# Performance work log

Measured on AMD Instinct MI355X. Metric: run time of the kernel, lower is better.

Reference implementation:

```python
import jax, jax.numpy as jnp
import numpy as np

DIM = 1024
NUM_HEADS = 16
NUM_GROUPS = 8


def setup_inputs() -> dict:
    key = jax.random.key(0)
    k1, k2, k3, k4 = jax.random.split(key, 4)
    B, L = 4, 4096
    x = jax.random.normal(k1, (B, L, DIM), dtype=jnp.float32)
    # torch Linear weights: [out_features, in_features]
    w_qkv = jax.random.normal(k2, (3 * DIM, DIM), dtype=jnp.float32) * (DIM ** -0.5)
    w_out = jax.random.normal(k3, (DIM, DIM), dtype=jnp.float32) * (DIM ** -0.5)
    b_out = jax.random.normal(k4, (DIM,), dtype=jnp.float32) * 0.01
    return {"x": x, "w_qkv": w_qkv, "w_out": w_out, "b_out": b_out}


def reference(x, w_qkv, w_out, b_out):
    B, L, D = x.shape
    H, G = NUM_HEADS, NUM_GROUPS
    dh = D // H
    lg = L // G  # block length per group
    # fused QKV projection (no bias)
    qkv = x @ w_qkv.T  # [B, L, 3D]
    qkv = qkv.reshape(B, L, 3, H, dh)
    qkv = jnp.transpose(qkv, (2, 0, 3, 1, 4))  # [3, B, H, L, dh]
    q, k, v = qkv[0], qkv[1], qkv[2]
    # group sequence into G blocks of length lg; attention within each block
    q = q.reshape(B, H, G, lg, dh)
    k = k.reshape(B, H, G, lg, dh)
    v = v.reshape(B, H, G, lg, dh)
    scale = dh ** -0.5
    scores = jnp.einsum('bhgld,bhgmd->bhglm', q, k) * scale  # [B,H,G,lg,lg]
    attn = jax.nn.softmax(scores, axis=-1)
    out = jnp.einsum('bhglm,bhgmd->bhgld', attn, v)  # [B,H,G,lg,dh]
    # 'b h g l d -> b (g l) (h d)'
    out = jnp.transpose(out, (0, 2, 3, 1, 4)).reshape(B, L, D)
    return out @ w_out.T + b_out
```

## Files before the change

kernel.cpp:

```cpp
#include <hip/hip_runtime.h>
#include <hip/hip_bf16.h>
#include <stdint.h>

typedef __bf16 bf16_t;
typedef __bf16 bf16x4 __attribute__((ext_vector_type(4)));
typedef __bf16 bf16x8 __attribute__((ext_vector_type(8)));
typedef float floatx4 __attribute__((ext_vector_type(4)));

#define MFMA_16x16x32_BF16(a, b, c) __builtin_amdgcn_mfma_f32_16x16x32_bf16((a), (b), (c), 0, 0, 0)

__device__ __forceinline__ void gload_lds16(const bf16_t* g, bf16_t* lds_base) {
  __builtin_amdgcn_global_load_lds(
      (const __attribute__((address_space(1))) void*)g,
      (__attribute__((address_space(3))) void*)lds_base, 16, 0, 0);
}

__global__ __launch_bounds__(256)
void f32_to_bf16_kernel(const float* __restrict__ in, bf16_t* __restrict__ out, int n8)
{
  for (int i = blockIdx.x * 256 + threadIdx.x; i < n8; i += gridDim.x * 256) {
    const float* p = in + (size_t)i * 8;
    floatx4 f0 = *(const floatx4*)p;
    floatx4 f1 = *(const floatx4*)(p + 4);
    bf16x8 r;
#pragma unroll
    for (int j = 0; j < 4; j++) { r[j] = (bf16_t)f0[j]; r[j + 4] = (bf16_t)f1[j]; }
    *(bf16x8*)(out + (size_t)i * 8) = r;
  }
}

template <typename TOUT, bool BIAS>
__global__ __launch_bounds__(512, 1)
void gemm_bt256(const bf16_t* __restrict__ A, const bf16_t* __restrict__ B,
                const float* __restrict__ bias, TOUT* __restrict__ C,
                int M, int N, int K)
{
  __shared__ bf16_t S[65536];
  const int t = threadIdx.x;
  const int lane = t & 63, wave = t >> 6;
  const int quad = lane >> 4, l15 = lane & 15;
  const int wm = wave >> 2, wn = wave & 3;

  const int cpx = gridDim.x >> 3;
  const int obid = blockIdx.x;
  const int bid = (obid & 7) * cpx + (obid >> 3);
  const int nbx = N >> 8;
  const int bx = bid % nbx, by = bid / nbx;
  const int m0 = by * 256, n0 = bx * 256;

  uint32_t aoff[4], boff[4];
  bf16_t* asd[4]; bf16_t* bsd[4];
#pragma unroll
  for (int j = 0; j < 4; j++) {
    const uint32_t o = (uint32_t)(j * 512 + t) * 16u;
    const uint32_t u = o ^ (((o >> 7) & 7u) << 4);
    const uint32_t row = u >> 7, colb = u & 127u;
    aoff[j] = (uint32_t)(m0 + row) * (uint32_t)(K * 2) + colb;
    boff[j] = (uint32_t)(n0 + row) * (uint32_t)(K * 2) + colb;
    asd[j] = S + j * 4096 + wave * 512;
    bsd[j] = S + 32768 + j * 4096 + wave * 512;
  }

  const uint32_t sw = (uint32_t)((l15 & 7) << 4);
  const uint32_t ce0 = (((uint32_t)(quad * 16)) ^ sw) >> 1;
  const uint32_t ce1 = ce0 ^ 32u;
  const bf16_t* lraA0 = S + (wm * 128 + l15) * 64 + ce0;
  const bf16_t* lraA1 = S + (wm * 128 + l15) * 64 + ce1;
  const bf16_t* lraB0 = S + 32768 + (wn * 64 + l15) * 64 + ce0;
  const bf16_t* lraB1 = S + 32768 + (wn * 64 + l15) * 64 + ce1;

  floatx4 acc[8][4] = {};

  const int NT = K >> 6;
#pragma unroll
  for (int j = 0; j < 4; j++) gload_lds16((const bf16_t*)((const char*)A + aoff[j]), asd[j]);
#pragma unroll
  for (int j = 0; j < 4; j++) gload_lds16((const bf16_t*)((const char*)B + boff[j]), bsd[j]);
#pragma unroll
  for (int j = 0; j < 4; j++) gload_lds16((const bf16_t*)((const char*)A + aoff[j] + 128), asd[j] + 16384);
#pragma unroll
  for (int j = 0; j < 4; j++) gload_lds16((const bf16_t*)((const char*)B + boff[j] + 128), bsd[j] + 16384);

  for (int kt = 0; kt < NT; kt++) {
    const int bo = (kt & 1) * 16384;
    if (kt < NT - 1) asm volatile("s_waitcnt vmcnt(8)" ::: "memory");
    else             asm volatile("s_waitcnt vmcnt(0)" ::: "memory");
    __builtin_amdgcn_s_barrier();
    __builtin_amdgcn_sched_barrier(0);

    bf16x8 af[4][2], bA[2][2], bB[2][2];
#pragma unroll
    for (int mi = 0; mi < 4; mi++) {
      af[mi][0] = *(const bf16x8*)(lraA0 + bo + mi * 1024);
      af[mi][1] = *(const bf16x8*)(lraA1 + bo + mi * 1024);
    }
#pragma unroll
    for (int ni = 0; ni < 2; ni++) {
      bA[ni][0] = *(const bf16x8*)(lraB0 + bo + ni * 1024);
      bA[ni][1] = *(const bf16x8*)(lraB1 + bo + ni * 1024);
    }
    __builtin_amdgcn_s_setprio(1);
#pragma unroll
    for (int mi = 0; mi < 4; mi++)
#pragma unroll
      for (int ni = 0; ni < 2; ni++) {
        acc[mi][ni] = MFMA_16x16x32_BF16(af[mi][0], bA[ni][0], acc[mi][ni]);
        acc[mi][ni] = MFMA_16x16x32_BF16(af[mi][1], bA[ni][1], acc[mi][ni]);
      }
    __builtin_amdgcn_s_setprio(0);
#pragma unroll
    for (int ni = 0; ni < 2; ni++) {
      bB[ni][0] = *(const bf16x8*)(lraB0 + bo + (ni + 2) * 1024);
      bB[ni][1] = *(const bf16x8*)(lraB1 + bo + (ni + 2) * 1024);
    }
    __builtin_amdgcn_s_setprio(1);
#pragma unroll
    for (int mi = 0; mi < 4; mi++)
#pragma unroll
      for (int ni = 0; ni < 2; ni++) {
        acc[mi][ni + 2] = MFMA_16x16x32_BF16(af[mi][0], bB[ni][0], acc[mi][ni + 2]);
        acc[mi][ni + 2] = MFMA_16x16x32_BF16(af[mi][1], bB[ni][1], acc[mi][ni + 2]);
      }
    __builtin_amdgcn_s_setprio(0);
#pragma unroll
    for (int mi = 0; mi < 4; mi++) {
      af[mi][0] = *(const bf16x8*)(lraA0 + bo + (mi + 4) * 1024);
      af[mi][1] = *(const bf16x8*)(lraA1 + bo + (mi + 4) * 1024);
    }
    __builtin_amdgcn_s_setprio(1);
#pragma unroll
    for (int mi = 0; mi < 4; mi++)
#pragma unroll
      for (int ni = 0; ni < 2; ni++) {
        acc[mi + 4][ni + 2] = MFMA_16x16x32_BF16(af[mi][0], bB[ni][0], acc[mi + 4][ni + 2]);
        acc[mi + 4][ni + 2] = MFMA_16x16x32_BF16(af[mi][1], bB[ni][1], acc[mi + 4][ni + 2]);
      }
    __builtin_amdgcn_s_setprio(0);
    __builtin_amdgcn_sched_barrier(0);
    __builtin_amdgcn_s_barrier();
    __builtin_amdgcn_sched_barrier(0);
    if (kt + 2 < NT) {
      const uint32_t kadv = (uint32_t)((kt + 2) * 128);
#pragma unroll
      for (int j = 0; j < 4; j++)
        gload_lds16((const bf16_t*)((const char*)A + aoff[j] + kadv), asd[j] + bo);
#pragma unroll
      for (int j = 0; j < 4; j++)
        gload_lds16((const bf16_t*)((const char*)B + boff[j] + kadv), bsd[j] + bo);
    }
    __builtin_amdgcn_s_setprio(1);
#pragma unroll
    for (int mi = 0; mi < 4; mi++)
#pragma unroll
      for (int ni = 0; ni < 2; ni++) {
        acc[mi + 4][ni] = MFMA_16x16x32_BF16(af[mi][0], bA[ni][0], acc[mi + 4][ni]);
        acc[mi + 4][ni] = MFMA_16x16x32_BF16(af[mi][1], bA[ni][1], acc[mi + 4][ni]);
      }
    __builtin_amdgcn_s_setprio(0);
  }

  if constexpr (sizeof(TOUT) == 2) {
    __syncthreads();
    bf16_t* Sw = S + wave * 1024;
#pragma unroll
    for (int mi = 0; mi < 8; mi++) {
#pragma unroll
      for (int ni = 0; ni < 4; ni++) {
        const int col = ((ni ^ quad) & 3) * 16 + l15;
        const float bv = BIAS ? bias[n0 + wn * 64 + ni * 16 + l15] : 0.0f;
#pragma unroll
        for (int r = 0; r < 4; r++)
          Sw[(quad * 4 + r) * 64 + col] = (bf16_t)(acc[mi][ni][r] + bv);
      }
#pragma unroll
      for (int c = 0; c < 2; c++) {
        const int idx = c * 64 + lane;
        const int row = idx >> 3, cg = idx & 7;
        const int scol = (cg * 8) ^ (((row >> 2) & 3) << 4);
        bf16x8 vrow = *(const bf16x8*)(Sw + row * 64 + scol);
        bf16_t* dst = (bf16_t*)C + (size_t)(m0 + wm * 128 + mi * 16 + row) * N
                      + (n0 + wn * 64 + cg * 8);
        *(bf16x8*)dst = vrow;
      }
    }
  } else {
#pragma unroll
    for (int ni = 0; ni < 4; ni++) {
      const int col = n0 + wn * 64 + ni * 16 + l15;
      const float bv = BIAS ? bias[col] : 0.0f;
#pragma unroll
      for (int mi = 0; mi < 8; mi++) {
        const size_t rbase = (size_t)(m0 + wm * 128 + mi * 16 + quad * 4) * N + col;
#pragma unroll
        for (int r = 0; r < 4; r++)
          C[rbase + (size_t)r * N] = (TOUT)(acc[mi][ni][r] + bv);
      }
    }
  }
}

__global__ __launch_bounds__(256)
void attn_kernel(const bf16_t* __restrict__ qkv, bf16_t* __restrict__ out)
{
  constexpr int VS = 72;
  __shared__ bf16_t Ks[64 * VS];
  __shared__ bf16_t Vt[64 * VS];
  __shared__ bf16_t Ps[4][16 * VS];

  const int h     = blockIdx.x & 15;
  const int qtile = blockIdx.x >> 4;

  const int t = threadIdx.x;
  const int wave = t >> 6, lane = t & 63;
  const int quad = lane >> 4, l15 = lane & 15;

  const int qrow0 = qtile * 256 + wave * 64;
  const int krow0 = (qtile >> 1) * 512;
  const int qcol = h * 64;
  const int kcol = 1024 + h * 64;
  const int vcol = 2048 + h * 64;

  bf16x8 qf[4][2];
#pragma unroll
  for (int mi = 0; mi < 4; mi++)
#pragma unroll
    for (int kb = 0; kb < 2; kb++)
      qf[mi][kb] = *(const bf16x8*)(qkv + (size_t)(qrow0 + mi * 16 + l15) * 3072 + qcol + kb * 32 + quad * 8);

  floatx4 o[4][4] = {};
  float plsum[4] = {};

  const float SCL = 0.125f * 1.44269504088896f;

  const bf16_t* kg0 = qkv + (size_t)(krow0 + (t >> 3)) * 3072 + kcol + (t & 7) * 8;
  const bf16_t* kg1 = qkv + (size_t)(krow0 + 32 + (t >> 3)) * 3072 + kcol + (t & 7) * 8;
  const bf16_t* vg0 = qkv + (size_t)(krow0 + (t & 63)) * 3072 + vcol + (t >> 6) * 8;
  const bf16_t* vg1 = qkv + (size_t)(krow0 + (t & 63)) * 3072 + vcol + ((t >> 6) + 4) * 8;
  bf16_t* ksd0 = Ks + (t >> 3) * VS + (t & 7) * 8;
  bf16_t* ksd1 = Ks + ((t >> 3) + 32) * VS + (t & 7) * 8;
  bf16_t* vtd0 = Vt + (t >> 6) * 8 * VS + (t & 63);
  bf16_t* vtd1 = Vt + ((t >> 6) + 4) * 8 * VS + (t & 63);

  bf16x8 kreg0 = *(const bf16x8*)kg0;
  bf16x8 kreg1 = *(const bf16x8*)kg1;
  bf16x8 vreg0 = *(const bf16x8*)vg0;
  bf16x8 vreg1 = *(const bf16x8*)vg1;

  for (int it = 0; it < 8; it++) {
    __syncthreads();
    *(bf16x8*)ksd0 = kreg0;
    *(bf16x8*)ksd1 = kreg1;
#pragma unroll
    for (int j = 0; j < 8; j++) { vtd0[j * VS] = vreg0[j]; vtd1[j * VS] = vreg1[j]; }
    __syncthreads();

    if (it < 7) {
      const size_t off = (size_t)(it + 1) * 64 * 3072;
      kreg0 = *(const bf16x8*)(kg0 + off);
      kreg1 = *(const bf16x8*)(kg1 + off);
      vreg0 = *(const bf16x8*)(vg0 + off);
      vreg1 = *(const bf16x8*)(vg1 + off);
    }

    bf16x8 kf[4][2], vf[4][2];
#pragma unroll
    for (int ni = 0; ni < 4; ni++)
#pragma unroll
      for (int kb = 0; kb < 2; kb++) {
        kf[ni][kb] = *(const bf16x8*)(Ks + (ni * 16 + l15) * VS + kb * 32 + quad * 8);
        vf[ni][kb] = *(const bf16x8*)(Vt + (ni * 16 + l15) * VS + kb * 32 + quad * 8);
      }

#pragma unroll
    for (int mi = 0; mi < 4; mi++) {
      floatx4 s[4] = {};
      __builtin_amdgcn_s_setprio(1);
#pragma unroll
      for (int ni = 0; ni < 4; ni++) {
        s[ni] = MFMA_16x16x32_BF16(kf[ni][0], qf[mi][0], s[ni]);
        s[ni] = MFMA_16x16x32_BF16(kf[ni][1], qf[mi][1], s[ni]);
      }
      __builtin_amdgcn_s_setprio(0);
      float ps = 0.0f;
#pragma unroll
      for (int ni = 0; ni < 4; ni++) {
        bf16x4 w;
#pragma unroll
        for (int r = 0; r < 4; r++) {
          const float p = exp2f(s[ni][r] * SCL);
          ps += p;
          w[r] = (bf16_t)p;
        }
        *(bf16x4*)(Ps[wave] + l15 * VS + ni * 16 + quad * 4) = w;
      }
      plsum[mi] += ps;
      bf16x8 pf0 = *(const bf16x8*)(Ps[wave] + l15 * VS + quad * 8);
      bf16x8 pf1 = *(const bf16x8*)(Ps[wave] + l15 * VS + 32 + quad * 8);
      __builtin_amdgcn_s_setprio(1);
#pragma unroll
      for (int ni = 0; ni < 4; ni++) {
        o[mi][ni] = MFMA_16x16x32_BF16(pf0, vf[ni][0], o[mi][ni]);
        o[mi][ni] = MFMA_16x16x32_BF16(pf1, vf[ni][1], o[mi][ni]);
      }
      __builtin_amdgcn_s_setprio(0);
    }
  }

#pragma unroll
  for (int mi = 0; mi < 4; mi++) {
    float tot = plsum[mi];
    tot += __shfl_xor(tot, 16, 64);
    tot += __shfl_xor(tot, 32, 64);
    const float inv = 1.0f / tot;
#pragma unroll
    for (int r = 0; r < 4; r++) {
      const float invr = __shfl(inv, quad * 4 + r, 16);
      const size_t rbase = (size_t)(qrow0 + mi * 16 + quad * 4 + r) * 1024 + h * 64 + l15;
#pragma unroll
      for (int ni = 0; ni < 4; ni++)
        out[rbase + ni * 16] = (bf16_t)(o[mi][ni][r] * invr);
    }
  }
}

extern "C" void kernel_launch(void* const* d_in, const int* in_sizes, int n_in,
                              void* d_out, int out_size, void* d_ws, size_t ws_size,
                              hipStream_t stream)
{
  const float* x     = (const float*)d_in[0];
  const float* w_qkv = (const float*)d_in[1];
  const float* w_out = (const float*)d_in[2];
  const float* b_out = (const float*)d_in[3];
  float* out = (float*)d_out;

  const size_t WQ = (size_t)3072 * 1024, WO = (size_t)1024 * 1024;
  bf16_t* wq_b = (bf16_t*)d_ws;
  bf16_t* wo_b = wq_b + WQ;

  int rows = 16384;
  while ((size_t)rows * 10240 + (WQ + WO) * 2 > ws_size && rows > 512) rows >>= 1;
  const int nchunk = 16384 / rows;

  bf16_t* qkv_c = wo_b + WO;
  bf16_t* att_c = qkv_c + (size_t)rows * 3072;
  bf16_t* x_c   = att_c + (size_t)rows * 1024;

  f32_to_bf16_kernel<<<1536, 256, 0, stream>>>(w_qkv, wq_b, (int)(WQ / 8));
  f32_to_bf16_kernel<<<512, 256, 0, stream>>>(w_out, wo_b, (int)(WO / 8));

  for (int c = 0; c < nchunk; c++) {
    const float* xc = x + (size_t)c * rows * 1024;
    float* outc = out + (size_t)c * rows * 1024;
    f32_to_bf16_kernel<<<2048, 256, 0, stream>>>(xc, x_c, rows * 128);
    gemm_bt256<bf16_t, false><<<dim3((3072 / 256) * (rows / 256)), 512, 0, stream>>>(
        x_c, wq_b, nullptr, qkv_c, rows, 3072, 1024);
    attn_kernel<<<dim3(16 * (rows / 256)), 256, 0, stream>>>(qkv_c, att_c);
    gemm_bt256<float, true><<<dim3((1024 / 256) * (rows / 256)), 512, 0, stream>>>(
        att_c, wo_b, b_out, outc, rows, 1024, 1024);
  }
}
```

Measured before the change: 362.8 us.

## Unroll GEMM main loop by two and prefetch next tile's fragments across barrier

```diff
diff --git a/kernel.cpp b/kernel.cpp
--- a/kernel.cpp
+++ b/kernel.cpp
@@ -70,94 +70,186 @@
   const bf16_t* lraB1 = S + 32768 + (wn * 64 + l15) * 64 + ce1;
 
   floatx4 acc[8][4] = {};
-
   const int NT = K >> 6;
-#pragma unroll
-  for (int j = 0; j < 4; j++) gload_lds16((const bf16_t*)((const char*)A + aoff[j]), asd[j]);
-#pragma unroll
-  for (int j = 0; j < 4; j++) gload_lds16((const bf16_t*)((const char*)B + boff[j]), bsd[j]);
-#pragma unroll
-  for (int j = 0; j < 4; j++) gload_lds16((const bf16_t*)((const char*)A + aoff[j] + 128), asd[j] + 16384);
-#pragma unroll
-  for (int j = 0; j < 4; j++) gload_lds16((const bf16_t*)((const char*)B + boff[j] + 128), bsd[j] + 16384);
-
-  for (int kt = 0; kt < NT; kt++) {
-    const int bo = (kt & 1) * 16384;
-    if (kt < NT - 1) asm volatile("s_waitcnt vmcnt(8)" ::: "memory");
-    else             asm volatile("s_waitcnt vmcnt(0)" ::: "memory");
+
+#define STAGE_TILE(kt, bo_) do {                                              \
+    const uint32_t kadv_ = (uint32_t)((kt) * 128);                            \
+    _Pragma("unroll")                                                         \
+    for (int j = 0; j < 4; j++)                                               \
+      gload_lds16((const bf16_t*)((const char*)A + aoff[j] + kadv_), asd[j] + (bo_)); \
+    _Pragma("unroll")                                                         \
+    for (int j = 0; j < 4; j++)                                               \
+      gload_lds16((const bf16_t*)((const char*)B + boff[j] + kadv_), bsd[j] + (bo_)); \
+  } while (0)
+
+#define FENCE() __builtin_amdgcn_sched_barrier(0)
+
+  bf16x8 afA[4][2];
+  bf16x8 afB[4][2];
+  bf16x8 bA[2][2];
+  bf16x8 bAn[2][2];
+  bf16x8 bB[2][2];
+
+  STAGE_TILE(0, 0);
+  STAGE_TILE(1, 16384);
+  asm volatile("s_waitcnt vmcnt(8)" ::: "memory");
+  __builtin_amdgcn_s_barrier();
+  FENCE();
+#pragma unroll
+  for (int mi = 0; mi < 4; mi++) {
+    afA[mi][0] = *(const bf16x8*)(lraA0 + mi * 1024);
+    afA[mi][1] = *(const bf16x8*)(lraA1 + mi * 1024);
+  }
+#pragma unroll
+  for (int ni = 0; ni < 2; ni++) {
+    bA[ni][0] = *(const bf16x8*)(lraB0 + ni * 1024);
+    bA[ni][1] = *(const bf16x8*)(lraB1 + ni * 1024);
+  }
+
+  for (int i = 0; ; i++) {
+    const int e = 2 * i;
+    __builtin_amdgcn_s_setprio(1);
+#pragma unroll
+    for (int mi = 0; mi < 4; mi++)
+#pragma unroll
+      for (int ni = 0; ni < 2; ni++) {
+        acc[mi][ni] = MFMA_16x16x32_BF16(afA[mi][0], bA[ni][0], acc[mi][ni]);
+        acc[mi][ni] = MFMA_16x16x32_BF16(afA[mi][1], bA[ni][1], acc[mi][ni]);
+      }
+    __builtin_amdgcn_s_setprio(0);
+#pragma unroll
+    for (int ni = 0; ni < 2; ni++) {
+      bB[ni][0] = *(const bf16x8*)(lraB0 + (ni + 2) * 1024);
+      bB[ni][1] = *(const bf16x8*)(lraB1 + (ni + 2) * 1024);
+    }
+    __builtin_amdgcn_s_setprio(1);
+#pragma unroll
+    for (int mi = 0; mi < 4; mi++)
+#pragma unroll
+      for (int ni = 0; ni < 2; ni++) {
+        acc[mi][ni + 2] = MFMA_16x16x32_BF16(afA[mi][0], bB[ni][0], acc[mi][ni + 2]);
+        acc[mi][ni + 2] = MFMA_16x16x32_BF16(afA[mi][1], bB[ni][1], acc[mi][ni + 2]);
+      }
+    __builtin_amdgcn_s_setprio(0);
+#pragma unroll
+    for (int mi = 0; mi < 4; mi++) {
+      afB[mi][0] = *(const bf16x8*)(lraA0 + (mi + 4) * 1024);
+      afB[mi][1] = *(const bf16x8*)(lraA1 + (mi + 4) * 1024);
+    }
+    __builtin_amdgcn_s_setprio(1);
+#pragma unroll
+    for (int mi = 0; mi < 4; mi++)
+#pragma unroll
+      for (int ni = 0; ni < 2; ni++) {
+        acc[mi + 4][ni + 2] = MFMA_16x16x32_BF16(afB[mi][0], bB[ni][0], acc[mi + 4][ni + 2]);
+        acc[mi + 4][ni + 2] = MFMA_16x16x32_BF16(afB[mi][1], bB[ni][1], acc[mi + 4][ni + 2]);
+      }
+    __builtin_amdgcn_s_setprio(0);
+    FENCE();
     __builtin_amdgcn_s_barrier();
-    __builtin_amdgcn_sched_barrier(0);
-
-    bf16x8 af[4][2], bA[2][2], bB[2][2];
+    FENCE();
+    if (e + 2 < NT) {
+      STAGE_TILE(e + 2, 0);
+      asm volatile("s_waitcnt vmcnt(8)" ::: "memory");
+    } else {
+      asm volatile("s_waitcnt vmcnt(0)" ::: "memory");
+    }
+    __builtin_amdgcn_s_barrier();
+    FENCE();
 #pragma unroll
     for (int mi = 0; mi < 4; mi++) {
-      af[mi][0] = *(const bf16x8*)(lraA0 + bo + mi * 1024);
-      af[mi][1] = *(const bf16x8*)(lraA1 + bo + mi * 1024);
+      afA[mi][0] = *(const bf16x8*)(lraA0 + 16384 + mi * 1024);
+      afA[mi][1] = *(const bf16x8*)(lraA1 + 16384 + mi * 1024);
     }
 #pragma unroll
     for (int ni = 0; ni < 2; ni++) {
-      bA[ni][0] = *(const bf16x8*)(lraB0 + bo + ni * 1024);
-      bA[ni][1] = *(const bf16x8*)(lraB1 + bo + ni * 1024);
-    }
-    __builtin_amdgcn_s_setprio(1);
-#pragma unroll
-    for (int mi = 0; mi < 4; mi++)
-#pragma unroll
-      for (int ni = 0; ni < 2; ni++) {
-        acc[mi][ni] = MFMA_16x16x32_BF16(af[mi][0], bA[ni][0], acc[mi][ni]);
-        acc[mi][ni] = MFMA_16x16x32_BF16(af[mi][1], bA[ni][1], acc[mi][ni]);
+      bAn[ni][0] = *(const bf16x8*)(lraB0 + 16384 + ni * 1024);
+      bAn[ni][1] = *(const bf16x8*)(lraB1 + 16384 + ni * 1024);
+    }
+    __builtin_amdgcn_s_setprio(1);
+#pragma unroll
+    for (int mi = 0; mi < 4; mi++)
+#pragma unroll
+      for (int ni = 0; ni < 2; ni++) {
+        acc[mi + 4][ni] = MFMA_16x16x32_BF16(afB[mi][0], bA[ni][0], acc[mi + 4][ni]);
+        acc[mi + 4][ni] = MFMA_16x16x32_BF16(afB[mi][1], bA[ni][1], acc[mi + 4][ni]);
+      }
+    __builtin_amdgcn_s_setprio(0);
+
+    __builtin_amdgcn_s_setprio(1);
+#pragma unroll
+    for (int mi = 0; mi < 4; mi++)
+#pragma unroll
+      for (int ni = 0; ni < 2; ni++) {
+        acc[mi][ni] = MFMA_16x16x32_BF16(afA[mi][0], bAn[ni][0], acc[mi][ni]);
+        acc[mi][ni] = MFMA_16x16x32_BF16(afA[mi][1], bAn[ni][1], acc[mi][ni]);
       }
     __builtin_amdgcn_s_setprio(0);
 #pragma unroll
     for (int ni = 0; ni < 2; ni++) {
-      bB[ni][0] = *(const bf16x8*)(lraB0 + bo + (ni + 2) * 1024);
-      bB[ni][1] = *(const bf16x8*)(lraB1 + bo + (ni + 2) * 1024);
-    }
-    __builtin_amdgcn_s_setprio(1);
-#pragma unroll
-    for (int mi = 0; mi < 4; mi++)
-#pragma unroll
-      for (int ni = 0; ni < 2; ni++) {
-        acc[mi][ni + 2] = MFMA_16x16x32_BF16(af[mi][0], bB[ni][0], acc[mi][ni + 2]);
-        acc[mi][ni + 2] = MFMA_16x16x32_BF16(af[mi][1], bB[ni][1], acc[mi][ni + 2]);
+      bB[ni][0] = *(const bf16x8*)(lraB0 + 16384 + (ni + 2) * 1024);
+      bB[ni][1] = *(const bf16x8*)(lraB1 + 16384 + (ni + 2) * 1024);
+    }
+    __builtin_amdgcn_s_setprio(1);
+#pragma unroll
+    for (int mi = 0; mi < 4; mi++)
+#pragma unroll
+      for (int ni = 0; ni < 2; ni++) {
+        acc[mi][ni + 2] = MFMA_16x16x32_BF16(afA[mi][0], bB[ni][0], acc[mi][ni + 2]);
+        acc[mi][ni + 2] = MFMA_16x16x32_BF16(afA[mi][1], bB[ni][1], acc[mi][ni + 2]);
       }
     __builtin_amdgcn_s_setprio(0);
 #pragma unroll
     for (int mi = 0; mi < 4; mi++) {
-      af[mi][0] = *(const bf16x8*)(lraA0 + bo + (mi + 4) * 1024);
-      af[mi][1] = *(const bf16x8*)(lraA1 + bo + (mi + 4) * 1024);
-    }
-    __builtin_amdgcn_s_setprio(1);
-#pragma unroll
-    for (int mi = 0; mi < 4; mi++)
-#pragma unroll
-      for (int ni = 0; ni < 2; ni++) {
-        acc[mi + 4][ni + 2] = MFMA_16x16x32_BF16(af[mi][0], bB[ni][0], acc[mi + 4][ni + 2]);
-        acc[mi + 4][ni + 2] = MFMA_16x16x32_BF16(af[mi][1], bB[ni][1], acc[mi + 4][ni + 2]);
-      }
-    __builtin_amdgcn_s_setprio(0);
-    __builtin_amdgcn_sched_barrier(0);
+      afB[mi][0] = *(const bf16x8*)(lraA0 + 16384 + (mi + 4) * 1024);
+      afB[mi][1] = *(const bf16x8*)(lraA1 + 16384 + (mi + 4) * 1024);
+    }
+    __builtin_amdgcn_s_setprio(1);
+#pragma unroll
+    for (int mi = 0; mi < 4; mi++)
+#pragma unroll
+      for (int ni = 0; ni < 2; ni++) {
+        acc[mi + 4][ni + 2] = MFMA_16x16x32_BF16(afB[mi][0], bB[ni][0], acc[mi + 4][ni + 2]);
+        acc[mi + 4][ni + 2] = MFMA_16x16x32_BF16(afB[mi][1], bB[ni][1], acc[mi + 4][ni + 2]);
+      }
+    __builtin_amdgcn_s_setprio(0);
+    FENCE();
     __builtin_amdgcn_s_barrier();
-    __builtin_amdgcn_sched_barrier(0);
-    if (kt + 2 < NT) {
-      const uint32_t kadv = (uint32_t)((kt + 2) * 128);
-#pragma unroll
-      for (int j = 0; j < 4; j++)
-        gload_lds16((const bf16_t*)((const char*)A + aoff[j] + kadv), asd[j] + bo);
-#pragma unroll
-      for (int j = 0; j < 4; j++)
-        gload_lds16((const bf16_t*)((const char*)B + boff[j] + kadv), bsd[j] + bo);
-    }
-    __builtin_amdgcn_s_setprio(1);
-#pragma unroll
-    for (int mi = 0; mi < 4; mi++)
-#pragma unroll
-      for (int ni = 0; ni < 2; ni++) {
-        acc[mi + 4][ni] = MFMA_16x16x32_BF16(af[mi][0], bA[ni][0], acc[mi + 4][ni]);
-        acc[mi + 4][ni] = MFMA_16x16x32_BF16(af[mi][1], bA[ni][1], acc[mi + 4][ni]);
-      }
-    __builtin_amdgcn_s_setprio(0);
-  }
+    FENCE();
+    const bool more = (e + 2) < NT;
+    if (e + 3 < NT) {
+      STAGE_TILE(e + 3, 16384);
+      asm volatile("s_waitcnt vmcnt(8)" ::: "memory");
+    } else if (more) {
+      asm volatile("s_waitcnt vmcnt(0)" ::: "memory");
+    }
+    if (more) {
+      __builtin_amdgcn_s_barrier();
+      FENCE();
+#pragma unroll
+      for (int mi = 0; mi < 4; mi++) {
+        afA[mi][0] = *(const bf16x8*)(lraA0 + mi * 1024);
+        afA[mi][1] = *(const bf16x8*)(lraA1 + mi * 1024);
+      }
+#pragma unroll
+      for (int ni = 0; ni < 2; ni++) {
+        bA[ni][0] = *(const bf16x8*)(lraB0 + ni * 1024);
+        bA[ni][1] = *(const bf16x8*)(lraB1 + ni * 1024);
+      }
+    }
+    __builtin_amdgcn_s_setprio(1);
+#pragma unroll
+    for (int mi = 0; mi < 4; mi++)
+#pragma unroll
+      for (int ni = 0; ni < 2; ni++) {
+        acc[mi + 4][ni] = MFMA_16x16x32_BF16(afB[mi][0], bAn[ni][0], acc[mi + 4][ni]);
+        acc[mi + 4][ni] = MFMA_16x16x32_BF16(afB[mi][1], bAn[ni][1], acc[mi + 4][ni]);
+      }
+    __builtin_amdgcn_s_setprio(0);
+    if (!more) break;
+  }
+#undef STAGE_TILE
+#undef FENCE
 
   if constexpr (sizeof(TOUT) == 2) {
     __syncthreads();
```

Result: slower. 433.8 us (+19.6%).
